# Optimization experiments

Hardware: AMD Instinct MI355X
Metric: run time of the kernel (lower is better)

Reference implementation:

```python
import jax, jax.numpy as jnp
import numpy as np

N, E, F_IN, H, C = 50000, 800000, 128, 128, 64


def setup_inputs() -> dict:
    key = jax.random.key(0)
    ks = jax.random.split(key, 10)
    s = lambda f: np.float32(1.0 / np.sqrt(f))
    return {
        "x": jax.random.normal(ks[0], (N, F_IN), jnp.float32),
        "edge_index": jax.random.randint(ks[1], (2, E), 0, N, dtype=jnp.int64),
        # SAGEConv1: lin_l (on aggregated neighbors, with bias) + lin_r (on root, no bias)
        "W1l": jax.random.normal(ks[2], (F_IN, H), jnp.float32) * s(F_IN),
        "b1l": jnp.zeros((H,), jnp.float32),
        "W1r": jax.random.normal(ks[3], (F_IN, H), jnp.float32) * s(F_IN),
        # SAGEConv2
        "W2l": jax.random.normal(ks[4], (H, C), jnp.float32) * s(H),
        "b2l": jnp.zeros((C,), jnp.float32),
        "W2r": jax.random.normal(ks[5], (H, C), jnp.float32) * s(H),
        # GCNConv
        "Wg": jax.random.normal(ks[6], (C, C), jnp.float32) * s(C),
        "bg": jnp.zeros((C,), jnp.float32),
    }


def sage_conv(x, edge_index, Wl, bl, Wr):
    # PyG SAGEConv (mean aggr): out = lin_l(mean_{j in N(i)} x_j) + lin_r(x_i)
    n = x.shape[0]
    src, dst = edge_index[0], edge_index[1]
    agg = jax.ops.segment_sum(x[src], dst, num_segments=n)  # [N, F]
    cnt = jax.ops.segment_sum(jnp.ones((src.shape[0],), x.dtype), dst, num_segments=n)
    mean = agg / jnp.maximum(cnt, 1.0)[:, None]
    return mean @ Wl + bl + x @ Wr


def gcn_conv(x, edge_index, W, b):
    # PyG GCNConv: add self loops, symmetric normalization D^-1/2 A D^-1/2
    n = x.shape[0]
    loop = jnp.arange(n, dtype=edge_index.dtype)
    src = jnp.concatenate([edge_index[0], loop])
    dst = jnp.concatenate([edge_index[1], loop])
    deg = jax.ops.segment_sum(jnp.ones((src.shape[0],), x.dtype), dst, num_segments=n)
    dinv = jnp.where(deg > 0, jax.lax.rsqrt(jnp.maximum(deg, 1e-12)), 0.0)
    norm = dinv[src] * dinv[dst]  # [E+N]
    xw = x @ W
    out = jax.ops.segment_sum(xw[src] * norm[:, None], dst, num_segments=n)
    return out + b


def reference(x, edge_index, W1l, b1l, W1r, W2l, b2l, W2r, Wg, bg):
    h = jax.nn.relu(sage_conv(x, edge_index, W1l, b1l, W1r))
    # dropout is identity in eval mode
    h = sage_conv(h, edge_index, W2l, b2l, W2r)
    h = jax.nn.softmax(h, axis=1)  # activate='softmax'
    return gcn_conv(h, edge_index, Wg, bg)
```

## Files before the change

kernel.cpp:

```cpp
#include <hip/hip_runtime.h>
#include <hip/hip_fp16.h>
#include <math.h>


typedef __attribute__((ext_vector_type(8))) short bf16x8;
typedef __attribute__((ext_vector_type(4))) float f32x4;

__device__ inline unsigned short f32_bf16_hi(float f) {
    unsigned int u = __builtin_bit_cast(unsigned int, f);
    u = (u + 0x7FFFu + ((u >> 16) & 1u)) >> 16;
    return (unsigned short)u;
}
__device__ inline float bf16_to_f32(unsigned short h) {
    unsigned int u = ((unsigned int)h) << 16;
    return __builtin_bit_cast(float, u);
}

union H8 { float4 f4; __half2 h[4]; };

__global__ void count_kernel(const int* __restrict__ dst, int* __restrict__ off,
                             int E, int NB, int BK) {
    __shared__ int hist[256];
    int t = threadIdx.x;
    hist[t] = 0;
    __syncthreads();
    int base = blockIdx.x * 8192;
    for (int i = t; i < 8192; i += 256) {
        int e = base + i;
        if (e < E) atomicAdd(&hist[dst[e] >> 8], 1);
    }
    __syncthreads();
    if (t < BK) off[1 + t * NB + blockIdx.x] = hist[t];
    if (blockIdx.x == 0 && t == 0) off[0] = 0;
}

__global__ void scan_reduce_kernel(const int* __restrict__ data, int* __restrict__ bsum, int n) {
    __shared__ int red[256];
    int t = threadIdx.x;
    int base = blockIdx.x * 2048 + t * 8;
    int s = 0;
    if (base + 8 <= n) {
        int4 a = *(const int4*)(data + base);
        int4 b = *(const int4*)(data + base + 4);
        s = a.x + a.y + a.z + a.w + b.x + b.y + b.z + b.w;
    } else {
        for (int i = 0; i < 8; ++i)
            if (base + i < n) s += data[base + i];
    }
    red[t] = s;
    __syncthreads();
    for (int off = 128; off > 0; off >>= 1) {
        if (t < off) red[t] += red[t + off];
        __syncthreads();
    }
    if (t == 0) bsum[blockIdx.x] = red[0];
}

__global__ void scan_offsets_kernel(int* __restrict__ bsum, int B) {
    if (threadIdx.x == 0 && blockIdx.x == 0) {
        int run = 0;
        for (int i = 0; i < B; ++i) { int v = bsum[i]; bsum[i] = run; run += v; }
    }
}

__global__ void scan_final_kernel(int* __restrict__ data, const int* __restrict__ bsum, int n) {
    __shared__ int tsum[256];
    int t = threadIdx.x;
    int base = blockIdx.x * 2048 + t * 8;
    int v[8];
    int s = 0;
#pragma unroll
    for (int i = 0; i < 8; ++i) {
        v[i] = (base + i < n) ? data[base + i] : 0;
        s += v[i];
    }
    tsum[t] = s;
    for (int off = 1; off < 256; off <<= 1) {
        __syncthreads();
        int u = (t >= off) ? tsum[t - off] : 0;
        __syncthreads();
        tsum[t] += u;
    }
    __syncthreads();
    int run = bsum[blockIdx.x] + tsum[t] - s;
#pragma unroll
    for (int i = 0; i < 8; ++i) {
        run += v[i];
        if (base + i < n) data[base + i] = run;
    }
}

__global__ void partition_kernel(const int* __restrict__ src, const int* __restrict__ dst,
                                 const int* __restrict__ off, unsigned* __restrict__ ebuf,
                                 int E, int NB, int BK) {
    __shared__ int cur[256];
    int t = threadIdx.x;
    if (t < BK) cur[t] = off[t * NB + blockIdx.x];
    __syncthreads();
    int base = blockIdx.x * 8192;
    for (int i = t; i < 8192; i += 256) {
        int e = base + i;
        if (e < E) {
            int d = dst[e];
            int pos = atomicAdd(&cur[d >> 8], 1);
            ebuf[pos] = ((unsigned)src[e] << 8) | (unsigned)(d & 255);
        }
    }
}

__global__ void finalize_kernel(const unsigned* __restrict__ ebuf, const int* __restrict__ off,
                                int* __restrict__ col, int* __restrict__ rowptr,
                                float* __restrict__ dinv, int N, int NB, int E) {
    __shared__ int hist[256], scn[256], cur[256];
    int b = blockIdx.x, t = threadIdx.x;
    int base = off[b * NB];
    int end  = off[(b + 1) * NB];
    int M = end - base;
    hist[t] = 0;
    __syncthreads();
    for (int i = t; i < M; i += 256) atomicAdd(&hist[ebuf[base + i] & 255u], 1);
    __syncthreads();
    scn[t] = hist[t];
    for (int o = 1; o < 256; o <<= 1) {
        __syncthreads();
        int u = (t >= o) ? scn[t - o] : 0;
        __syncthreads();
        scn[t] += u;
    }
    __syncthreads();
    int excl = scn[t] - hist[t];
    int node = b * 256 + t;
    if (node < N) {
        rowptr[node] = base + excl;
        dinv[node] = rsqrtf((float)(hist[t] + 1));
    }
    if (b == 0 && t == 0) rowptr[N] = E;
    cur[t] = base + excl;
    __syncthreads();
    for (int i = t; i < M; i += 256) {
        unsigned w = ebuf[base + i];
        int pos = atomicAdd(&cur[w & 255u], 1);
        col[pos] = (int)(w >> 8);
    }
}

__global__ void packw_kernel(const float* __restrict__ W1l, const float* __restrict__ W1r,
                             const float* __restrict__ W2l, const float* __restrict__ W2r,
                             const float* __restrict__ Wg,
                             unsigned short* __restrict__ p1h, unsigned short* __restrict__ p1l,
                             unsigned short* __restrict__ p2h, unsigned short* __restrict__ p2l,
                             unsigned short* __restrict__ p3h, unsigned short* __restrict__ p3l) {
    int which = blockIdx.y;
    const float* W;
    unsigned short *hi, *lo;
    int K, Mp, colOff, T;
    if (which == 0)      { W = W1l; hi = p1h; lo = p1l; K = 128; Mp = 128; colOff = 0;   T = 16; }
    else if (which == 1) { W = W1r; hi = p1h; lo = p1l; K = 128; Mp = 128; colOff = 128; T = 16; }
    else if (which == 2) { W = W2l; hi = p2h; lo = p2l; K = 128; Mp = 64;  colOff = 0;   T = 8;  }
    else if (which == 3) { W = W2r; hi = p2h; lo = p2l; K = 128; Mp = 64;  colOff = 64;  T = 8;  }
    else                 { W = Wg;  hi = p3h; lo = p3l; K = 64;  Mp = 64;  colOff = 0;   T = 4;  }
    int idx = blockIdx.x * blockDim.x + threadIdx.x;
    if (idx >= K * Mp) return;
    int k = idx / Mp, m = idx % Mp;
    float w = W[(size_t)k * Mp + m];
    int colI = colOff + m;
    int s = k >> 5, kk = k & 31, qq = kk >> 3, j = kk & 7;
    int tt = colI >> 4, n = colI & 15;
    int lane = qq * 16 + n;
    size_t pos = ((size_t)(s * T + tt) * 64 + lane) * 8 + j;
    unsigned short h = f32_bf16_hi(w);
    hi[pos] = h;
    lo[pos] = f32_bf16_hi(w - bf16_to_f32(h));
}

__launch_bounds__(256)
__global__ void gemm1_kernel(const float* __restrict__ A,
                             const unsigned short* __restrict__ Whi,
                             const unsigned short* __restrict__ Wlo,
                             __half* __restrict__ outA, __half* __restrict__ outB, int N) {
    constexpr int Ttot = 16, TB = 8;
    const int lane = threadIdx.x & 63;
    const int wave = threadIdx.x >> 6;
    const int m = lane & 15, q = lane >> 4;
    const int t0 = blockIdx.y * TB;
    const int row0 = blockIdx.x * 64 + wave * 16;
    int arow = row0 + m;
    if (arow >= N) arow = N - 1;
    const float* ap = A + (size_t)arow * 128 + q * 8;

    float av[4][8];
#pragma unroll
    for (int s = 0; s < 4; ++s) {
        *(float4*)(av[s])     = *(const float4*)(ap + s * 32);
        *(float4*)(av[s] + 4) = *(const float4*)(ap + s * 32 + 4);
    }
    bf16x8 ahi[4], alo[4];
#pragma unroll
    for (int s = 0; s < 4; ++s)
#pragma unroll
        for (int i = 0; i < 8; ++i) {
            unsigned short h = f32_bf16_hi(av[s][i]);
            ahi[s][i] = (short)h;
            alo[s][i] = (short)f32_bf16_hi(av[s][i] - bf16_to_f32(h));
        }

    f32x4 acc[TB];
#pragma unroll
    for (int t = 0; t < TB; ++t) acc[t] = (f32x4)(0.f);
    const bf16x8* whp = (const bf16x8*)Whi;
    const bf16x8* wlp = (const bf16x8*)Wlo;
#pragma unroll
    for (int s = 0; s < 4; ++s) {
        const int base = (s * Ttot + t0) * 64 + lane;
#pragma unroll
        for (int t = 0; t < TB; ++t) {
            bf16x8 wh = whp[base + t * 64];
            bf16x8 wl = wlp[base + t * 64];
            acc[t] = __builtin_amdgcn_mfma_f32_16x16x32_bf16(ahi[s], wh, acc[t], 0, 0, 0);
            acc[t] = __builtin_amdgcn_mfma_f32_16x16x32_bf16(alo[s], wh, acc[t], 0, 0, 0);
            acc[t] = __builtin_amdgcn_mfma_f32_16x16x32_bf16(ahi[s], wl, acc[t], 0, 0, 0);
        }
    }

#pragma unroll
    for (int r = 0; r < 4; ++r) {
        int row = row0 + q * 4 + r;
        if (row < N) {
            __half* op = (blockIdx.y == 0) ? outA : outB;
#pragma unroll
            for (int t = 0; t < TB; ++t) {
                int c = (t0 + t) * 16 + m - blockIdx.y * 128;
                op[(size_t)row * 128 + c] = __float2half(acc[t][r]);
            }
        }
    }
}

__launch_bounds__(256)
__global__ void sage2_fused_kernel(const __half* __restrict__ p16, const __half* __restrict__ q16,
                                   const int* __restrict__ rowptr, const int* __restrict__ col,
                                   const float* __restrict__ b1l,
                                   const unsigned short* __restrict__ Whi,
                                   const unsigned short* __restrict__ Wlo,
                                   __half* __restrict__ r16, __half* __restrict__ s16, int N) {
    const int lane = threadIdx.x & 63;
    const int wave = threadIdx.x >> 6;
    const int m = lane & 15, q = lane >> 4;
    const int row0 = blockIdx.x * 64 + wave * 16;
    int node = row0 + m;
    int nclamp = (node < N) ? node : (N - 1);
    int sIdx = rowptr[nclamp];
    int eIdx = (node < N) ? rowptr[nclamp + 1] : sIdx;

    float acc[4][8];
#pragma unroll
    for (int s = 0; s < 4; ++s)
#pragma unroll
        for (int i = 0; i < 8; ++i) acc[s][i] = 0.f;

    const __half* pb = p16 + q * 8;
    int ptr = sIdx;
    for (; ptr + 4 <= eIdx; ptr += 4) {
        int j0 = col[ptr], j1 = col[ptr + 1], j2 = col[ptr + 2], j3 = col[ptr + 3];
        H8 u[4][4];
#pragma unroll
        for (int s = 0; s < 4; ++s) {
            u[0][s].f4 = *(const float4*)(pb + (size_t)j0 * 128 + s * 32);
            u[1][s].f4 = *(const float4*)(pb + (size_t)j1 * 128 + s * 32);
            u[2][s].f4 = *(const float4*)(pb + (size_t)j2 * 128 + s * 32);
            u[3][s].f4 = *(const float4*)(pb + (size_t)j3 * 128 + s * 32);
        }
#pragma unroll
        for (int s = 0; s < 4; ++s)
#pragma unroll
            for (int k = 0; k < 4; ++k) {
                float2 f0 = __half22float2(u[0][s].h[k]);
                float2 f1 = __half22float2(u[1][s].h[k]);
                float2 f2 = __half22float2(u[2][s].h[k]);
                float2 f3 = __half22float2(u[3][s].h[k]);
                acc[s][2 * k]     += (f0.x + f1.x) + (f2.x + f3.x);
                acc[s][2 * k + 1] += (f0.y + f1.y) + (f2.y + f3.y);
            }
    }
    for (; ptr < eIdx; ++ptr) {
        int j0 = col[ptr];
#pragma unroll
        for (int s = 0; s < 4; ++s) {
            H8 u0;
            u0.f4 = *(const float4*)(pb + (size_t)j0 * 128 + s * 32);
#pragma unroll
            for (int k = 0; k < 4; ++k) {
                float2 f0 = __half22float2(u0.h[k]);
                acc[s][2 * k]     += f0.x;
                acc[s][2 * k + 1] += f0.y;
            }
        }
    }

    float inv = 1.0f / fmaxf((float)(eIdx - sIdx), 1.0f);
    bf16x8 ahi[4], alo[4];
#pragma unroll
    for (int s = 0; s < 4; ++s) {
        H8 qv;
        qv.f4 = *(const float4*)(q16 + (size_t)nclamp * 128 + s * 32 + q * 8);
        float bv[8];
        *(float4*)(bv)     = *(const float4*)(b1l + s * 32 + q * 8);
        *(float4*)(bv + 4) = *(const float4*)(b1l + s * 32 + q * 8 + 4);
#pragma unroll
        for (int i = 0; i < 8; ++i) {
            float qf = __half2float(((const __half*)&qv)[i]);
            float h = fmaxf(acc[s][i] * inv + qf + bv[i], 0.f);
            unsigned short hb = f32_bf16_hi(h);
            ahi[s][i] = (short)hb;
            alo[s][i] = (short)f32_bf16_hi(h - bf16_to_f32(hb));
        }
    }

    f32x4 accm[8];
#pragma unroll
    for (int t = 0; t < 8; ++t) accm[t] = (f32x4)(0.f);
    const bf16x8* whp = (const bf16x8*)Whi;
    const bf16x8* wlp = (const bf16x8*)Wlo;
#pragma unroll
    for (int s = 0; s < 4; ++s) {
        const int base = (s * 8) * 64 + lane;
#pragma unroll
        for (int t = 0; t < 8; ++t) {
            bf16x8 wh = whp[base + t * 64];
            bf16x8 wl = wlp[base + t * 64];
            accm[t] = __builtin_amdgcn_mfma_f32_16x16x32_bf16(ahi[s], wh, accm[t], 0, 0, 0);
            accm[t] = __builtin_amdgcn_mfma_f32_16x16x32_bf16(alo[s], wh, accm[t], 0, 0, 0);
            accm[t] = __builtin_amdgcn_mfma_f32_16x16x32_bf16(ahi[s], wl, accm[t], 0, 0, 0);
        }
    }
#pragma unroll
    for (int r = 0; r < 4; ++r) {
        int row = row0 + q * 4 + r;
        if (row < N) {
#pragma unroll
            for (int t = 0; t < 8; ++t) {
                int c = t * 16 + m;
                float v = accm[t][r];
                if (c < 64) r16[(size_t)row * 64 + c] = __float2half(v);
                else        s16[(size_t)row * 64 + (c - 64)] = __float2half(v);
            }
        }
    }
}

__launch_bounds__(256)
__global__ void gcn_prep_fused_kernel(const __half* __restrict__ r16, const __half* __restrict__ s16,
                                      const int* __restrict__ rowptr, const int* __restrict__ col,
                                      const float* __restrict__ b2l,
                                      const unsigned short* __restrict__ Whi,
                                      const unsigned short* __restrict__ Wlo,
                                      const float* __restrict__ dinv,
                                      __half* __restrict__ tp16, int N) {
    const int lane = threadIdx.x & 63;
    const int wave = threadIdx.x >> 6;
    const int m = lane & 15, q = lane >> 4;
    const int row0 = blockIdx.x * 64 + wave * 16;
    int node = row0 + m;
    int nclamp = (node < N) ? node : (N - 1);
    int sIdx = rowptr[nclamp];
    int eIdx = (node < N) ? rowptr[nclamp + 1] : sIdx;

    float acc[2][8];
#pragma unroll
    for (int s = 0; s < 2; ++s)
#pragma unroll
        for (int i = 0; i < 8; ++i) acc[s][i] = 0.f;

    const __half* rb = r16 + q * 8;
    int ptr = sIdx;
    for (; ptr + 4 <= eIdx; ptr += 4) {
        int j0 = col[ptr], j1 = col[ptr + 1], j2 = col[ptr + 2], j3 = col[ptr + 3];
        H8 u[4][2];
#pragma unroll
        for (int s = 0; s < 2; ++s) {
            u[0][s].f4 = *(const float4*)(rb + (size_t)j0 * 64 + s * 32);
            u[1][s].f4 = *(const float4*)(rb + (size_t)j1 * 64 + s * 32);
            u[2][s].f4 = *(const float4*)(rb + (size_t)j2 * 64 + s * 32);
            u[3][s].f4 = *(const float4*)(rb + (size_t)j3 * 64 + s * 32);
        }
#pragma unroll
        for (int s = 0; s < 2; ++s)
#pragma unroll
            for (int k = 0; k < 4; ++k) {
                float2 f0 = __half22float2(u[0][s].h[k]);
                float2 f1 = __half22float2(u[1][s].h[k]);
                float2 f2 = __half22float2(u[2][s].h[k]);
                float2 f3 = __half22float2(u[3][s].h[k]);
                acc[s][2 * k]     += (f0.x + f1.x) + (f2.x + f3.x);
                acc[s][2 * k + 1] += (f0.y + f1.y) + (f2.y + f3.y);
            }
    }
    for (; ptr < eIdx; ++ptr) {
        int j0 = col[ptr];
#pragma unroll
        for (int s = 0; s < 2; ++s) {
            H8 u0;
            u0.f4 = *(const float4*)(rb + (size_t)j0 * 64 + s * 32);
#pragma unroll
            for (int k = 0; k < 4; ++k) {
                float2 f0 = __half22float2(u0.h[k]);
                acc[s][2 * k]     += f0.x;
                acc[s][2 * k + 1] += f0.y;
            }
        }
    }

    float inv = 1.0f / fmaxf((float)(eIdx - sIdx), 1.0f);
    float v[2][8];
    float mx = -1e30f;
#pragma unroll
    for (int s = 0; s < 2; ++s) {
        H8 sv;
        sv.f4 = *(const float4*)(s16 + (size_t)nclamp * 64 + s * 32 + q * 8);
        float bv[8];
        *(float4*)(bv)     = *(const float4*)(b2l + s * 32 + q * 8);
        *(float4*)(bv + 4) = *(const float4*)(b2l + s * 32 + q * 8 + 4);
#pragma unroll
        for (int i = 0; i < 8; ++i) {
            float sf = __half2float(((const __half*)&sv)[i]);
            v[s][i] = acc[s][i] * inv + sf + bv[i];
            mx = fmaxf(mx, v[s][i]);
        }
    }
    mx = fmaxf(mx, __shfl_xor(mx, 16, 64));
    mx = fmaxf(mx, __shfl_xor(mx, 32, 64));
    float sm = 0.f;
#pragma unroll
    for (int s = 0; s < 2; ++s)
#pragma unroll
        for (int i = 0; i < 8; ++i) {
            v[s][i] = expf(v[s][i] - mx);
            sm += v[s][i];
        }
    sm += __shfl_xor(sm, 16, 64);
    sm += __shfl_xor(sm, 32, 64);
    float is = 1.0f / sm;

    bf16x8 ahi[2], alo[2];
#pragma unroll
    for (int s = 0; s < 2; ++s)
#pragma unroll
        for (int i = 0; i < 8; ++i) {
            float h = v[s][i] * is;
            unsigned short hb = f32_bf16_hi(h);
            ahi[s][i] = (short)hb;
            alo[s][i] = (short)f32_bf16_hi(h - bf16_to_f32(hb));
        }

    f32x4 accm[4];
#pragma unroll
    for (int t = 0; t < 4; ++t) accm[t] = (f32x4)(0.f);
    const bf16x8* whp = (const bf16x8*)Whi;
    const bf16x8* wlp = (const bf16x8*)Wlo;
#pragma unroll
    for (int s = 0; s < 2; ++s) {
        const int base = (s * 4) * 64 + lane;
#pragma unroll
        for (int t = 0; t < 4; ++t) {
            bf16x8 wh = whp[base + t * 64];
            bf16x8 wl = wlp[base + t * 64];
            accm[t] = __builtin_amdgcn_mfma_f32_16x16x32_bf16(ahi[s], wh, accm[t], 0, 0, 0);
            accm[t] = __builtin_amdgcn_mfma_f32_16x16x32_bf16(alo[s], wh, accm[t], 0, 0, 0);
            accm[t] = __builtin_amdgcn_mfma_f32_16x16x32_bf16(ahi[s], wl, accm[t], 0, 0, 0);
        }
    }
#pragma unroll
    for (int r = 0; r < 4; ++r) {
        int row = row0 + q * 4 + r;
        if (row < N) {
            float sc = dinv[row];
#pragma unroll
            for (int t = 0; t < 4; ++t) {
                int c = t * 16 + m;
                tp16[(size_t)row * 64 + c] = __float2half(accm[t][r] * sc);
            }
        }
    }
}

__global__ void gcn_agg_kernel(const __half* __restrict__ tp,
                               const int* __restrict__ rowptr, const int* __restrict__ col,
                               const float* __restrict__ dinv, const float* __restrict__ bg,
                               float* __restrict__ out, int N) {
    int node = blockIdx.x * 4 + (threadIdx.x >> 6);
    if (node >= N) return;
    int lane = threadIdx.x & 63;
    int s = rowptr[node], e = rowptr[node + 1];
    float a[8];
#pragma unroll
    for (int k = 0; k < 8; ++k) a[k] = 0.f;
    int p = s;
    for (; p + 8 <= e; p += 8) {
#pragma unroll
        for (int k = 0; k < 8; ++k)
            a[k] += __half2float(tp[(size_t)col[p + k] * 64 + lane]);
    }
    for (; p < e; ++p) a[0] += __half2float(tp[(size_t)col[p] * 64 + lane]);
    float acc = ((a[0] + a[1]) + (a[2] + a[3])) + ((a[4] + a[5]) + (a[6] + a[7]));
    float di = dinv[node];
    out[(size_t)node * 64 + lane] =
        (acc + __half2float(tp[(size_t)node * 64 + lane])) * di + bg[lane];
}

extern "C" void kernel_launch(void* const* d_in, const int* in_sizes, int n_in,
                              void* d_out, int out_size, void* d_ws, size_t ws_size,
                              hipStream_t stream) {
    const float* x = (const float*)d_in[0];
    const int* ei = (const int*)d_in[1];
    const float* W1l = (const float*)d_in[2];
    const float* b1l = (const float*)d_in[3];
    const float* W1r = (const float*)d_in[4];
    const float* W2l = (const float*)d_in[5];
    const float* b2l = (const float*)d_in[6];
    const float* W2r = (const float*)d_in[7];
    const float* Wg  = (const float*)d_in[8];
    const float* bg  = (const float*)d_in[9];

    const int N = in_sizes[0] / 128;
    const int E = in_sizes[1] / 2;
    const int* srcp = ei;
    const int* dstp = ei + E;

    const int NB = (E + 8191) / 8192;
    const int BK = (N + 255) >> 8;
    const int len = BK * NB;

    float* ws = (float*)d_ws;
    float* dinv = ws;
    __half* p16 = (__half*)(dinv + N);
    __half* q16 = p16 + (size_t)N * 128;
    __half* r16 = q16 + (size_t)N * 128;
    __half* s16 = r16 + (size_t)N * 64;
    __half* tp16 = s16 + (size_t)N * 64;
    int* rowptr = (int*)(tp16 + (size_t)N * 64);
    int* off    = rowptr + (N + 1);
    int* colbuf = off + len + 2;
    unsigned* ebuf = (unsigned*)(colbuf + E);
    int* bsum   = (int*)(ebuf + E);
    uintptr_t up = (uintptr_t)(bsum + 32);
    up = (up + 15) & ~(uintptr_t)15;
    unsigned short* p1h = (unsigned short*)up;
    unsigned short* p1l = p1h + 32768;
    unsigned short* p2h = p1l + 32768;
    unsigned short* p2l = p2h + 16384;
    unsigned short* p3h = p2l + 16384;
    unsigned short* p3l = p3h + 4096;

    float* out = (float*)d_out;

    count_kernel<<<NB, 256, 0, stream>>>(dstp, off, E, NB, BK);
    const int sn = len + 1;
    const int SBs = (sn + 2047) / 2048;
    scan_reduce_kernel<<<SBs, 256, 0, stream>>>(off, bsum, sn);
    scan_offsets_kernel<<<1, 64, 0, stream>>>(bsum, SBs);
    scan_final_kernel<<<SBs, 256, 0, stream>>>(off, bsum, sn);
    partition_kernel<<<NB, 256, 0, stream>>>(srcp, dstp, off, ebuf, E, NB, BK);
    finalize_kernel<<<BK, 256, 0, stream>>>(ebuf, off, colbuf, rowptr, dinv, N, NB, E);

    packw_kernel<<<dim3(64, 5), 256, 0, stream>>>(W1l, W1r, W2l, W2r, Wg,
                                                  p1h, p1l, p2h, p2l, p3h, p3l);

    const int gb = (N + 63) / 64;
    const int ab = (N + 3) / 4;

    gemm1_kernel<<<dim3(gb, 2), 256, 0, stream>>>(x, p1h, p1l, p16, q16, N);

    sage2_fused_kernel<<<gb, 256, 0, stream>>>(p16, q16, rowptr, colbuf, b1l,
                                               p2h, p2l, r16, s16, N);

    gcn_prep_fused_kernel<<<gb, 256, 0, stream>>>(r16, s16, rowptr, colbuf, b2l,
                                                  p3h, p3l, dinv, tp16, N);

    gcn_agg_kernel<<<ab, 256, 0, stream>>>(tp16, rowptr, colbuf, dinv, bg, out, N);
}
```

Measured before the change: 285.7 us.

## Split neighbor gather across wave pairs and vectorize GCN aggregation lanes

In the two fused SAGE/GCN-prep kernels, each 16-row group is now handled by a pair of waves. Each wave gathers half of every node's neighbor list, the partial sums are combined through swizzled shared memory, and each wave then computes half of the output columns with MFMA. This doubles the grid and shortens the serial gather chain per wave, at the cost of LDS traffic and block-level barriers. The final GCN aggregation now processes two edges per step using half2 loads across the two half-waves, then reduces them with a cross-lane shuffle.

```diff
diff --git a/kernel.cpp b/kernel.cpp
--- a/kernel.cpp
+++ b/kernel.cpp
@@ -243,14 +243,21 @@
                                    const unsigned short* __restrict__ Whi,
                                    const unsigned short* __restrict__ Wlo,
                                    __half* __restrict__ r16, __half* __restrict__ s16, int N) {
+    __shared__ float part[4][64][16];
     const int lane = threadIdx.x & 63;
     const int wave = threadIdx.x >> 6;
+    const int pairH = wave & 1;
+    const int grp   = wave >> 1;
     const int m = lane & 15, q = lane >> 4;
-    const int row0 = blockIdx.x * 64 + wave * 16;
+    const int row0 = blockIdx.x * 32 + grp * 16;
     int node = row0 + m;
     int nclamp = (node < N) ? node : (N - 1);
-    int sIdx = rowptr[nclamp];
-    int eIdx = (node < N) ? rowptr[nclamp + 1] : sIdx;
+    int sAll = rowptr[nclamp];
+    int eAll = (node < N) ? rowptr[nclamp + 1] : sAll;
+    int deg  = eAll - sAll;
+    int half0 = (deg + 1) >> 1;
+    int sIdx = sAll + (pairH ? half0 : 0);
+    int eIdx = pairH ? eAll : (sAll + half0);
 
     float acc[4][8];
 #pragma unroll
@@ -297,7 +304,28 @@
         }
     }
 
-    float inv = 1.0f / fmaxf((float)(eIdx - sIdx), 1.0f);
+    float* ap = &acc[0][0];
+    const int swz = lane & 3;
+#pragma unroll
+    for (int c = 0; c < 2; ++c) {
+        if (c) __syncthreads();
+#pragma unroll
+        for (int sl = 0; sl < 4; ++sl)
+            *(float4*)&part[wave][lane][(sl ^ swz) * 4] =
+                *(const float4*)(ap + (c * 4 + sl) * 4);
+        __syncthreads();
+#pragma unroll
+        for (int sl = 0; sl < 4; ++sl) {
+            float4 pv = *(const float4*)&part[wave ^ 1][lane][(sl ^ swz) * 4];
+            int g = (c * 4 + sl) * 4;
+            ap[g]     += pv.x;
+            ap[g + 1] += pv.y;
+            ap[g + 2] += pv.z;
+            ap[g + 3] += pv.w;
+        }
+    }
+
+    float inv = 1.0f / fmaxf((float)deg, 1.0f);
     bf16x8 ahi[4], alo[4];
 #pragma unroll
     for (int s = 0; s < 4; ++s) {
@@ -316,16 +344,16 @@
         }
     }
 
-    f32x4 accm[8];
-#pragma unroll
-    for (int t = 0; t < 8; ++t) accm[t] = (f32x4)(0.f);
+    f32x4 accm[4];
+#pragma unroll
+    for (int t = 0; t < 4; ++t) accm[t] = (f32x4)(0.f);
     const bf16x8* whp = (const bf16x8*)Whi;
     const bf16x8* wlp = (const bf16x8*)Wlo;
 #pragma unroll
     for (int s = 0; s < 4; ++s) {
-        const int base = (s * 8) * 64 + lane;
-#pragma unroll
-        for (int t = 0; t < 8; ++t) {
+        const int base = (s * 8 + pairH * 4) * 64 + lane;
+#pragma unroll
+        for (int t = 0; t < 4; ++t) {
             bf16x8 wh = whp[base + t * 64];
             bf16x8 wl = wlp[base + t * 64];
             accm[t] = __builtin_amdgcn_mfma_f32_16x16x32_bf16(ahi[s], wh, accm[t], 0, 0, 0);
@@ -333,16 +361,15 @@
             accm[t] = __builtin_amdgcn_mfma_f32_16x16x32_bf16(ahi[s], wl, accm[t], 0, 0, 0);
         }
     }
+    __half* op = pairH ? s16 : r16;
 #pragma unroll
     for (int r = 0; r < 4; ++r) {
         int row = row0 + q * 4 + r;
         if (row < N) {
 #pragma unroll
-            for (int t = 0; t < 8; ++t) {
+            for (int t = 0; t < 4; ++t) {
                 int c = t * 16 + m;
-                float v = accm[t][r];
-                if (c < 64) r16[(size_t)row * 64 + c] = __float2half(v);
-                else        s16[(size_t)row * 64 + (c - 64)] = __float2half(v);
+                op[(size_t)row * 64 + c] = __float2half(accm[t][r]);
             }
         }
     }
@@ -356,14 +383,21 @@
                                       const unsigned short* __restrict__ Wlo,
                                       const float* __restrict__ dinv,
                                       __half* __restrict__ tp16, int N) {
+    __shared__ float part[4][64][16];
     const int lane = threadIdx.x & 63;
     const int wave = threadIdx.x >> 6;
+    const int pairH = wave & 1;
+    const int grp   = wave >> 1;
     const int m = lane & 15, q = lane >> 4;
-    const int row0 = blockIdx.x * 64 + wave * 16;
+    const int row0 = blockIdx.x * 32 + grp * 16;
     int node = row0 + m;
     int nclamp = (node < N) ? node : (N - 1);
-    int sIdx = rowptr[nclamp];
-    int eIdx = (node < N) ? rowptr[nclamp + 1] : sIdx;
+    int sAll = rowptr[nclamp];
+    int eAll = (node < N) ? rowptr[nclamp + 1] : sAll;
+    int deg  = eAll - sAll;
+    int half0 = (deg + 1) >> 1;
+    int sIdx = sAll + (pairH ? half0 : 0);
+    int eIdx = pairH ? eAll : (sAll + half0);
 
     float acc[2][8];
 #pragma unroll
@@ -410,7 +444,22 @@
         }
     }
 
-    float inv = 1.0f / fmaxf((float)(eIdx - sIdx), 1.0f);
+    float* ap = &acc[0][0];
+    const int swz = lane & 3;
+#pragma unroll
+    for (int sl = 0; sl < 4; ++sl)
+        *(float4*)&part[wave][lane][(sl ^ swz) * 4] = *(const float4*)(ap + sl * 4);
+    __syncthreads();
+#pragma unroll
+    for (int sl = 0; sl < 4; ++sl) {
+        float4 pv = *(const float4*)&part[wave ^ 1][lane][(sl ^ swz) * 4];
+        ap[sl * 4]     += pv.x;
+        ap[sl * 4 + 1] += pv.y;
+        ap[sl * 4 + 2] += pv.z;
+        ap[sl * 4 + 3] += pv.w;
+    }
+
+    float inv = 1.0f / fmaxf((float)deg, 1.0f);
     float v[2][8];
     float mx = -1e30f;
 #pragma unroll
@@ -452,16 +501,16 @@
             alo[s][i] = (short)f32_bf16_hi(h - bf16_to_f32(hb));
         }
 
-    f32x4 accm[4];
-#pragma unroll
-    for (int t = 0; t < 4; ++t) accm[t] = (f32x4)(0.f);
+    f32x4 accm[2];
+#pragma unroll
+    for (int t = 0; t < 2; ++t) accm[t] = (f32x4)(0.f);
     const bf16x8* whp = (const bf16x8*)Whi;
     const bf16x8* wlp = (const bf16x8*)Wlo;
 #pragma unroll
     for (int s = 0; s < 2; ++s) {
-        const int base = (s * 4) * 64 + lane;
-#pragma unroll
-        for (int t = 0; t < 4; ++t) {
+        const int base = (s * 4 + pairH * 2) * 64 + lane;
+#pragma unroll
+        for (int t = 0; t < 2; ++t) {
             bf16x8 wh = whp[base + t * 64];
             bf16x8 wl = wlp[base + t * 64];
             accm[t] = __builtin_amdgcn_mfma_f32_16x16x32_bf16(ahi[s], wh, accm[t], 0, 0, 0);
@@ -475,8 +524,8 @@
         if (row < N) {
             float sc = dinv[row];
 #pragma unroll
-            for (int t = 0; t < 4; ++t) {
-                int c = t * 16 + m;
+            for (int t = 0; t < 2; ++t) {
+                int c = (pairH * 2 + t) * 16 + m;
                 tp16[(size_t)row * 64 + c] = __float2half(accm[t][r] * sc);
             }
         }
@@ -490,21 +539,40 @@
     int node = blockIdx.x * 4 + (threadIdx.x >> 6);
     if (node >= N) return;
     int lane = threadIdx.x & 63;
+    int f2 = lane & 31;
+    int ep = lane >> 5;
     int s = rowptr[node], e = rowptr[node + 1];
-    float a[8];
-#pragma unroll
-    for (int k = 0; k < 8; ++k) a[k] = 0.f;
+    float ax[8], ay[8];
+#pragma unroll
+    for (int k = 0; k < 8; ++k) { ax[k] = 0.f; ay[k] = 0.f; }
     int p = s;
-    for (; p + 8 <= e; p += 8) {
-#pragma unroll
-        for (int k = 0; k < 8; ++k)
-            a[k] += __half2float(tp[(size_t)col[p + k] * 64 + lane]);
-    }
-    for (; p < e; ++p) a[0] += __half2float(tp[(size_t)col[p] * 64 + lane]);
-    float acc = ((a[0] + a[1]) + (a[2] + a[3])) + ((a[4] + a[5]) + (a[6] + a[7]));
-    float di = dinv[node];
-    out[(size_t)node * 64 + lane] =
-        (acc + __half2float(tp[(size_t)node * 64 + lane])) * di + bg[lane];
+    for (; p + 16 <= e; p += 16) {
+#pragma unroll
+        for (int k = 0; k < 8; ++k) {
+            int j = col[p + 2 * k + ep];
+            float2 f = __half22float2(*(const __half2*)(tp + (size_t)j * 64 + 2 * f2));
+            ax[k] += f.x;
+            ay[k] += f.y;
+        }
+    }
+    for (int t = p + ep; t < e; t += 2) {
+        int j = col[t];
+        float2 f = __half22float2(*(const __half2*)(tp + (size_t)j * 64 + 2 * f2));
+        ax[0] += f.x;
+        ay[0] += f.y;
+    }
+    float sx = ((ax[0] + ax[1]) + (ax[2] + ax[3])) + ((ax[4] + ax[5]) + (ax[6] + ax[7]));
+    float sy = ((ay[0] + ay[1]) + (ay[2] + ay[3])) + ((ay[4] + ay[5]) + (ay[6] + ay[7]));
+    sx += __shfl_xor(sx, 32, 64);
+    sy += __shfl_xor(sy, 32, 64);
+    if (ep == 0) {
+        float2 selfv = __half22float2(*(const __half2*)(tp + (size_t)node * 64 + 2 * f2));
+        float di = dinv[node];
+        float2 o;
+        o.x = (sx + selfv.x) * di + bg[2 * f2];
+        o.y = (sy + selfv.y) * di + bg[2 * f2 + 1];
+        *(float2*)(out + (size_t)node * 64 + 2 * f2) = o;
+    }
 }
 
 extern "C" void kernel_launch(void* const* d_in, const int* in_sizes, int n_in,
@@ -565,16 +633,17 @@
     packw_kernel<<<dim3(64, 5), 256, 0, stream>>>(W1l, W1r, W2l, W2r, Wg,
                                                   p1h, p1l, p2h, p2l, p3h, p3l);
 
-    const int gb = (N + 63) / 64;
-    const int ab = (N + 3) / 4;
+    const int gb  = (N + 63) / 64;
+    const int gbf = (N + 31) / 32;
+    const int ab  = (N + 3) / 4;
 
     gemm1_kernel<<<dim3(gb, 2), 256, 0, stream>>>(x, p1h, p1l, p16, q16, N);
 
-    sage2_fused_kernel<<<gb, 256, 0, stream>>>(p16, q16, rowptr, colbuf, b1l,
-                                               p2h, p2l, r16, s16, N);
-
-    gcn_prep_fused_kernel<<<gb, 256, 0, stream>>>(r16, s16, rowptr, colbuf, b2l,
-                                                  p3h, p3l, dinv, tp16, N);
+    sage2_fused_kernel<<<gbf, 256, 0, stream>>>(p16, q16, rowptr, colbuf, b1l,
+                                                p2h, p2l, r16, s16, N);
+
+    gcn_prep_fused_kernel<<<gbf, 256, 0, stream>>>(r16, s16, rowptr, colbuf, b2l,
+                                                   p3h, p3l, dinv, tp16, N);
 
     gcn_agg_kernel<<<ab, 256, 0, stream>>>(tp16, rowptr, colbuf, dinv, bg, out, N);
 }
```

Measured after the change: 282.6 us. No clear change (-1.1%).
